# Performance work log

Hardware: AMD Instinct MI355X
Metric: run time of the kernel (lower is better)

Reference implementation:

```python
import jax, jax.numpy as jnp
import numpy as np

N, K, GDIM, DDIM, HID = 2000, 250, 256, 20, 150
GIJ = 3 * GDIM + DDIM  # 788
BINS = jnp.array([1, 2, 3, 4, 8, 16, 32, 64], dtype=jnp.int32)


def _pair_structure():
    # span i (1..N-1) has min(i, K) antecedents: spans i-L .. i-1
    lengths = np.minimum(np.arange(1, N), K)
    i_arr = np.repeat(np.arange(1, N), lengths)
    pos = np.concatenate([np.arange(L) for L in lengths])
    Lrep = np.repeat(lengths, lengths)
    j_arr = i_arr - Lrep + pos
    seg = np.repeat(np.arange(N - 1), lengths)
    # span k covers tokens [2k, 2k+1]; distance = i.i2 - j.i1
    dist = (2 * i_arr + 1) - 2 * j_arr
    return i_arr, j_arr, dist, seg, pos, lengths


def setup_inputs() -> dict:
    key = jax.random.key(0)
    ks = jax.random.split(key, 8)
    i_arr, j_arr, dist, seg, pos, lengths = _pair_structure()

    def w(k, shape, scale):
        return jax.random.normal(k, shape, dtype=jnp.float32) * scale

    return {
        "g_i": w(ks[0], (N, GDIM), 1.0),
        "mention_scores": w(ks[1], (N, 1), 1.0),
        "dist_embed": w(ks[2], (9, DDIM), 0.1),
        "W1": w(ks[3], (GIJ, HID), float(1.0 / np.sqrt(GIJ))),
        "b1": jnp.zeros((HID,), jnp.float32),
        "W2": w(ks[4], (HID, HID), float(1.0 / np.sqrt(HID))),
        "b2": jnp.zeros((HID,), jnp.float32),
        "W3": w(ks[5], (HID, 1), float(1.0 / np.sqrt(HID))),
        "b3": jnp.zeros((1,), jnp.float32),
        "mention_ids": jnp.asarray(i_arr, jnp.int32),
        "antecedent_ids": jnp.asarray(j_arr, jnp.int32),
        "distances": jnp.asarray(dist, jnp.int32),
        "seg_ids": jnp.asarray(seg, jnp.int32),
        "pos_ids": jnp.asarray(pos, jnp.int32),
        "lengths": jnp.asarray(lengths, jnp.int32),
    }


def reference(g_i, mention_scores, dist_embed, W1, b1, W2, b2, W3, b3,
              mention_ids, antecedent_ids, distances, seg_ids, pos_ids, lengths):
    # Distance.stoi: bin index = number of bins <= num; then embedding lookup
    dist_idx = jnp.sum(distances[:, None] >= BINS[None, :], axis=1)
    phi = dist_embed[dist_idx]                               # [P, DDIM]

    i_g = g_i[mention_ids]                                   # [P, GDIM]
    j_g = g_i[antecedent_ids]                                # [P, GDIM]
    pairs = jnp.concatenate([i_g, j_g, i_g * j_g, phi], axis=1)  # [P, GIJ]

    # Score MLP (dropout is identity in eval mode)
    h = jax.nn.relu(pairs @ W1 + b1)
    h = jax.nn.relu(h @ W2 + b2)
    s_ij = h @ W3 + b3                                       # [P, 1]

    coref = mention_scores[mention_ids] + mention_scores[antecedent_ids] + s_ij  # [P, 1]
    c = coref[:, 0]

    # ragged per-span softmax with appended epsilon (score 0), pad value 1000
    n_groups = lengths.shape[0]                              # N - 1 nonempty groups
    mat = jnp.full((n_groups, K + 1), -jnp.inf, dtype=c.dtype)
    mat = mat.at[seg_ids, pos_ids].set(c)
    mat = mat.at[jnp.arange(n_groups), lengths].set(0.0)     # epsilon slot
    probs_rows = jax.nn.softmax(mat, axis=1)                 # -inf -> prob 0
    valid = jnp.arange(K + 1)[None, :] <= lengths[:, None]
    probs_rows = jnp.where(valid, probs_rows, jnp.asarray(1000.0, c.dtype))
    # leading empty group: softmax([epsilon]) = [1.0], rest padded with 1000
    first = jnp.full((1, K + 1), 1000.0, dtype=c.dtype).at[0, 0].set(1.0)
    probs = jnp.concatenate([first, probs_rows], axis=0)     # [N, K+1]

    with_epsilon_my = jnp.concatenate([jnp.zeros_like(coref), coref], axis=1)  # [P, 2]
    return probs, with_epsilon_my
```

## Files before the change

kernel.cpp:

```cpp
#include <hip/hip_runtime.h>
#include <hip/hip_bf16.h>

#define GDIM 256
#define HID 150
#define HP 160
#define KMAX 250
#define NMAX 2000

typedef __attribute__((ext_vector_type(8))) short bf16x8;
typedef __attribute__((ext_vector_type(4))) float f32x4;

#define FU   0
#define FV   (FU + NMAX*HP)
#define FD   (FV + NMAX*HP)
#define FW3  (FD + 9*HP)
#define FB2  (FW3 + HP)
#define FEND (FB2 + HP)
#define CH_SH 5120
#define NCH1  8
#define NCH   13

static __device__ __forceinline__ short cvt_bf(float x) {
  __hip_bfloat16 h = __float2bfloat16(x);
  return *reinterpret_cast<short*>(&h);
}

static __device__ __forceinline__ void gl_lds16(const void* g, void* l) {
  __builtin_amdgcn_global_load_lds(
      (const __attribute__((address_space(1))) unsigned int*)g,
      (__attribute__((address_space(3))) unsigned int*)l, 16, 0, 0);
}

__global__ void precompute_uv(const float* __restrict__ g_i,
                              const float* __restrict__ W1,
                              const float* __restrict__ b1,
                              float* __restrict__ ws, int N) {
  int t = blockIdx.x * blockDim.x + threadIdx.x;
  int total = N * HP;
  bool isV = false;
  if (t >= total) { t -= total; isV = true; }
  if (t >= total) return;
  int r = t / HP, c = t - (t / HP) * HP;
  float acc = 0.f;
  if (c < HID) {
    const float* w = W1 + (isV ? GDIM * HID : 0) + c;
    const float* g = g_i + (size_t)r * GDIM;
#pragma unroll 8
    for (int k = 0; k < GDIM; k++) acc = fmaf(g[k], w[(size_t)k * HID], acc);
    if (!isV) acc += b1[c];
  }
  ws[(isV ? FV : FU) + (size_t)r * HP + c] = acc;
}

__global__ void precompute_tabs(const float* __restrict__ dist_embed,
                                const float* __restrict__ W1,
                                const float* __restrict__ W2,
                                const float* __restrict__ b2,
                                const float* __restrict__ W3,
                                float* __restrict__ wsf) {
  unsigned short* wsu = (unsigned short*)(wsf + FEND);
  int t = blockIdx.x * blockDim.x + threadIdx.x;
  if (t < 9 * HP) {
    int d = t / HP, c = t - d * HP;
    float a = 0.f;
    if (c < HID) {
#pragma unroll
      for (int k = 0; k < 20; k++)
        a = fmaf(dist_embed[d * 20 + k], W1[(size_t)(768 + k) * HID + c], a);
    }
    wsf[FD + t] = a;
    return;
  }
  t -= 9 * HP;
  if (t < HP) { wsf[FW3 + t] = (t < HID) ? W3[t] : 0.f; return; }
  t -= HP;
  if (t < HP) { wsf[FB2 + t] = (t < HID) ? b2[t] : 0.f; return; }
  t -= HP;
  if (t < NCH * CH_SH) {
    int ch = t / CH_SH, qs = t - ch * CH_SH;
    int s = qs >> 6, bs = qs & 63;
    int bbs = bs ^ ((s & 7) << 3);
    int n = 2 * s + (bbs >> 5);
    int kk = bbs & 31;
    float w = 0.f;
    if (ch < NCH1) {
      int k = ch * 32 + kk;
      if (n < HID) w = W1[(size_t)(2 * GDIM + k) * HID + n];
    } else {
      int k = (ch - NCH1) * 32 + kk;
      if (n < HID && k < HID) w = W2[(size_t)k * HID + n];
    }
    wsu[t] = (unsigned short)cvt_bf(w);
    return;
  }
}

__global__ __launch_bounds__(512, 4)
void pair_mlp(const float* __restrict__ g_i,
              const float* __restrict__ ms,
              const int* __restrict__ mid,
              const int* __restrict__ aid,
              const int* __restrict__ dist,
              const float* __restrict__ b3,
              const float* __restrict__ wsf,
              float* __restrict__ out2, int P) {
  __shared__ short Bb[2][CH_SH];
  __shared__ short Hh[8][2560];
  const unsigned short* wsu = (const unsigned short*)(wsf + FEND);

  int tid = threadIdx.x;
  int wave = tid >> 6, lane = tid & 63;
  int c = lane & 15, g = lane >> 4;
  int tbase = blockIdx.x * 128;

  int prow = tbase + wave * 16 + c;
  int pcA = (prow < P) ? prow : (P - 1);
  const float* gI = g_i + (size_t)mid[pcA] * GDIM;
  const float* gJ = g_i + (size_t)aid[pcA] * GDIM;

  int bOff[10];
#pragma unroll
  for (int ct = 0; ct < 10; ct++) {
    int n = 16 * ct + c;
    bOff[ct] = (n >> 1) * 128 + ((((n & 1) << 6) + g * 16) ^ (((n >> 1) & 7) << 4));
  }

  {
    const char* s = (const char*)(wsu);
    char* d = (char*)&Bb[0][0];
    gl_lds16(s + wave * 1024 + lane * 16, d + wave * 1024);
    if (wave < 2)
      gl_lds16(s + 8192 + wave * 1024 + lane * 16, d + 8192 + wave * 1024);
  }
  __syncthreads();

  f32x4 acc[10];
#pragma unroll
  for (int ct = 0; ct < 10; ct++) acc[ct] = (f32x4){0.f, 0.f, 0.f, 0.f};

  for (int t = 0; t < NCH1; t++) {
    {
      const char* s = (const char*)(wsu + (size_t)(t + 1) * CH_SH);
      char* d = (char*)&Bb[(t + 1) & 1][0];
      gl_lds16(s + wave * 1024 + lane * 16, d + wave * 1024);
      if (wave < 2)
        gl_lds16(s + 8192 + wave * 1024 + lane * 16, d + 8192 + wave * 1024);
    }
    int ko = t * 32 + g * 8;
    float4 i0 = *(const float4*)(gI + ko), i1 = *(const float4*)(gI + ko + 4);
    float4 j0 = *(const float4*)(gJ + ko), j1 = *(const float4*)(gJ + ko + 4);
    bf16x8 A;
    A[0] = cvt_bf(i0.x * j0.x); A[1] = cvt_bf(i0.y * j0.y);
    A[2] = cvt_bf(i0.z * j0.z); A[3] = cvt_bf(i0.w * j0.w);
    A[4] = cvt_bf(i1.x * j1.x); A[5] = cvt_bf(i1.y * j1.y);
    A[6] = cvt_bf(i1.z * j1.z); A[7] = cvt_bf(i1.w * j1.w);

    const char* Bp = (const char*)&Bb[t & 1][0];
#pragma unroll
    for (int ct = 0; ct < 10; ct++) {
      bf16x8 Bf = *(const bf16x8*)(Bp + bOff[ct]);
      acc[ct] = __builtin_amdgcn_mfma_f32_16x16x32_bf16(A, Bf, acc[ct], 0, 0, 0);
    }
    __syncthreads();
  }

  int im[4], jm[4], dm[4];
#pragma unroll
  for (int r = 0; r < 4; r++) {
    int p = tbase + wave * 16 + g * 4 + r;
    int pc = (p < P) ? p : (P - 1);
    im[r] = mid[pc]; jm[r] = aid[pc];
    int d = dist[pc];
    dm[r] = (d >= 1) + (d >= 2) + (d >= 3) + (d >= 4) +
            (d >= 8) + (d >= 16) + (d >= 32) + (d >= 64);
  }
  const float* Ut = wsf + FU;
  const float* Vt = wsf + FV;
  const float* Dt = wsf + FD;
  char* Hw = (char*)&Hh[wave][0];
#pragma unroll
  for (int ct = 0; ct < 10; ct++) {
#pragma unroll
    for (int r = 0; r < 4; r++) {
      int col = 16 * ct + c;
      float bias = Ut[(size_t)im[r] * HP + col] +
                   Vt[(size_t)jm[r] * HP + col] +
                   Dt[dm[r] * HP + col];
      float h = fmaxf(acc[ct][r] + bias, 0.f);
      int row = g * 4 + r;
      int byte = 32 * ct + 2 * c;
      int bo = (byte < 256) ? (byte ^ ((row & 7) << 4))
                            : (256 + ((byte - 256) ^ ((row & 3) << 4)));
      *(short*)(Hw + row * 320 + bo) = cvt_bf(h);
    }
  }

  f32x4 acc2[10];
#pragma unroll
  for (int ct = 0; ct < 10; ct++) acc2[ct] = (f32x4){0.f, 0.f, 0.f, 0.f};

  for (int t = NCH1; t < NCH; t++) {
    if (t + 1 < NCH) {
      const char* s = (const char*)(wsu + (size_t)(t + 1) * CH_SH);
      char* d = (char*)&Bb[(t + 1) & 1][0];
      gl_lds16(s + wave * 1024 + lane * 16, d + wave * 1024);
      if (wave < 2)
        gl_lds16(s + 8192 + wave * 1024 + lane * 16, d + 8192 + wave * 1024);
    }
    int ks = t - NCH1;
    int kbyte = ks * 64 + g * 16;
    int bo = (kbyte < 256) ? (kbyte ^ ((c & 7) << 4))
                           : (256 + ((kbyte - 256) ^ ((c & 3) << 4)));
    bf16x8 A2 = *(const bf16x8*)((const char*)&Hh[wave][0] + c * 320 + bo);

    const char* Bp = (const char*)&Bb[t & 1][0];
#pragma unroll
    for (int ct = 0; ct < 10; ct++) {
      bf16x8 Bf = *(const bf16x8*)(Bp + bOff[ct]);
      acc2[ct] = __builtin_amdgcn_mfma_f32_16x16x32_bf16(A2, Bf, acc2[ct], 0, 0, 0);
    }
    __syncthreads();
  }

  float b2v[10], w3v[10];
#pragma unroll
  for (int ct = 0; ct < 10; ct++) {
    b2v[ct] = wsf[FB2 + 16 * ct + c];
    w3v[ct] = wsf[FW3 + 16 * ct + c];
  }
  float b3v = b3[0];
#pragma unroll
  for (int r = 0; r < 4; r++) {
    float s = 0.f;
#pragma unroll
    for (int ct = 0; ct < 10; ct++) {
      float a = acc2[ct][r] + b2v[ct];
      s = fmaf(fmaxf(a, 0.f), w3v[ct], s);
    }
    s += __shfl_xor(s, 1, 64);
    s += __shfl_xor(s, 2, 64);
    s += __shfl_xor(s, 4, 64);
    s += __shfl_xor(s, 8, 64);
    if (c == 0) {
      int p = tbase + wave * 16 + g * 4 + r;
      if (p < P) {
        float val = s + ms[im[r]] + ms[jm[r]] + b3v;
        ((float2*)out2)[p] = make_float2(0.f, val);
      }
    }
  }
}

__global__ __launch_bounds__(64, 1)
void softmax_rows(const float* __restrict__ out2,
                  float* __restrict__ probs, int G) {
  int b = blockIdx.x;
  int t = threadIdx.x;
  if (b == 0) {
    for (int pos = t; pos <= KMAX; pos += 64)
      probs[pos] = (pos == 0) ? 1.0f : 1000.0f;
    return;
  }
  int g = b - 1;
  int L = (g + 1 < KMAX) ? g + 1 : KMAX;
  int base = (g <= KMAX) ? g * (g + 1) / 2
                         : KMAX * (KMAX + 1) / 2 + (g - KMAX) * KMAX;
  float mx = 0.f;
  for (int pos = t; pos < L; pos += 64)
    mx = fmaxf(mx, out2[2 * (base + pos) + 1]);
#pragma unroll
  for (int off = 32; off >= 1; off >>= 1) mx = fmaxf(mx, __shfl_xor(mx, off));

  float sum = (t == 0) ? expf(-mx) : 0.f;
  for (int pos = t; pos < L; pos += 64)
    sum += expf(out2[2 * (base + pos) + 1] - mx);
#pragma unroll
  for (int off = 32; off >= 1; off >>= 1) sum += __shfl_xor(sum, off);
  float inv = 1.f / sum;

  float* row = probs + (size_t)(g + 1) * (KMAX + 1);
  for (int pos = t; pos <= KMAX; pos += 64) {
    float v;
    if (pos < L)       v = expf(out2[2 * (base + pos) + 1] - mx) * inv;
    else if (pos == L) v = expf(-mx) * inv;
    else               v = 1000.0f;
    row[pos] = v;
  }
}

extern "C" void kernel_launch(void* const* d_in, const int* in_sizes, int n_in,
                              void* d_out, int out_size, void* d_ws, size_t ws_size,
                              hipStream_t stream) {
  const float* g_i        = (const float*)d_in[0];
  const float* ms         = (const float*)d_in[1];
  const float* dist_embed = (const float*)d_in[2];
  const float* W1         = (const float*)d_in[3];
  const float* b1         = (const float*)d_in[4];
  const float* W2         = (const float*)d_in[5];
  const float* b2         = (const float*)d_in[6];
  const float* W3         = (const float*)d_in[7];
  const float* b3         = (const float*)d_in[8];
  const int* mid          = (const int*)d_in[9];
  const int* aid          = (const int*)d_in[10];
  const int* dist         = (const int*)d_in[11];

  int N = in_sizes[0] / GDIM;
  int P = in_sizes[9];
  int G = in_sizes[14];

  float* wsf   = (float*)d_ws;
  float* probs = (float*)d_out;
  float* out2  = (float*)d_out + (size_t)(G + 1) * (KMAX + 1);

  int tot_uv = 2 * N * HP;
  precompute_uv<<<(tot_uv + 255) / 256, 256, 0, stream>>>(g_i, W1, b1, wsf, N);
  int tot_tab = 9 * HP + 2 * HP + NCH * CH_SH;
  precompute_tabs<<<(tot_tab + 255) / 256, 256, 0, stream>>>(dist_embed, W1, W2, b2, W3, wsf);
  pair_mlp<<<(P + 127) / 128, 512, 0, stream>>>(g_i, ms, mid, aid, dist, b3, wsf, out2, P);
  softmax_rows<<<G + 1, 64, 0, stream>>>(out2, probs, G);
}
```

Before: 352.7 us.

## Give each wave two M tiles with K=64 chunks and register prefetch

The pair MLP kernel moves from 8 waves that each own 16 rows to 4 waves that each own 32 rows (two M tiles), so every B fragment read from LDS feeds two MFMAs. Weight chunks grow to K=64 with a new swizzle, which halves the number of barrier-separated steps. The next chunk's g_i rows are prefetched into registers, and the MFMA loops are wrapped in s_setprio. precompute_uv also computes four columns per thread. The trade-off is higher register pressure and lower occupancy (256 threads, launch bounds 2), which may hurt latency hiding of the gather loads.

Result: faster. 295.8 us (-16.1%).

```diff
diff --git a/kernel.cpp b/kernel.cpp
--- a/kernel.cpp
+++ b/kernel.cpp
@@ -16,9 +16,8 @@
 #define FW3  (FD + 9*HP)
 #define FB2  (FW3 + HP)
 #define FEND (FB2 + HP)
-#define CH_SH 5120
-#define NCH1  8
-#define NCH   13
+#define CHFULL 10240
+#define UBTOT  66560
 
 static __device__ __forceinline__ short cvt_bf(float x) {
   __hip_bfloat16 h = __float2bfloat16(x);
@@ -29,6 +28,14 @@
   __builtin_amdgcn_global_load_lds(
       (const __attribute__((address_space(1))) unsigned int*)g,
       (__attribute__((address_space(3))) unsigned int*)l, 16, 0, 0);
+}
+
+static __device__ __forceinline__ void stage_chunk(const unsigned short* src, short* dst,
+                                                   int nseg, int wave, int lane) {
+  const char* s = (const char*)src;
+  char* d = (char*)dst;
+  for (int seg = wave; seg < nseg; seg += 4)
+    gl_lds16(s + seg * 1024 + lane * 16, d + seg * 1024);
 }
 
 __global__ void precompute_uv(const float* __restrict__ g_i,
@@ -36,20 +43,36 @@
                               const float* __restrict__ b1,
                               float* __restrict__ ws, int N) {
   int t = blockIdx.x * blockDim.x + threadIdx.x;
-  int total = N * HP;
+  int total = N * (HP / 4);
   bool isV = false;
   if (t >= total) { t -= total; isV = true; }
   if (t >= total) return;
-  int r = t / HP, c = t - (t / HP) * HP;
-  float acc = 0.f;
-  if (c < HID) {
-    const float* w = W1 + (isV ? GDIM * HID : 0) + c;
+  int r = t / (HP / 4), c4 = (t - r * (HP / 4)) * 4;
+  float a0 = 0.f, a1 = 0.f, a2 = 0.f, a3 = 0.f;
+  if (c4 < HID) {
+    const float* w = W1 + (isV ? GDIM * HID : 0) + c4;
     const float* g = g_i + (size_t)r * GDIM;
-#pragma unroll 8
-    for (int k = 0; k < GDIM; k++) acc = fmaf(g[k], w[(size_t)k * HID], acc);
-    if (!isV) acc += b1[c];
-  }
-  ws[(isV ? FV : FU) + (size_t)r * HP + c] = acc;
+#pragma unroll 4
+    for (int k = 0; k < GDIM; k++) {
+      float gv = g[k];
+      const float* wr = w + (size_t)k * HID;
+      a0 = fmaf(gv, wr[0], a0);
+      a1 = fmaf(gv, wr[1], a1);
+      a2 = fmaf(gv, wr[2], a2);
+      a3 = fmaf(gv, wr[3], a3);
+    }
+    if (!isV) {
+      a0 += b1[c4];
+      if (c4 + 1 < HID) a1 += b1[c4 + 1];
+      if (c4 + 2 < HID) a2 += b1[c4 + 2];
+      if (c4 + 3 < HID) a3 += b1[c4 + 3];
+    }
+  }
+  float* dst = ws + (isV ? FV : FU) + (size_t)r * HP + c4;
+  dst[0] = (c4     < HID) ? a0 : 0.f;
+  dst[1] = (c4 + 1 < HID) ? a1 : 0.f;
+  dst[2] = (c4 + 2 < HID) ? a2 : 0.f;
+  dst[3] = (c4 + 3 < HID) ? a3 : 0.f;
 }
 
 __global__ void precompute_tabs(const float* __restrict__ dist_embed,
@@ -76,18 +99,19 @@
   t -= HP;
   if (t < HP) { wsf[FB2 + t] = (t < HID) ? b2[t] : 0.f; return; }
   t -= HP;
-  if (t < NCH * CH_SH) {
-    int ch = t / CH_SH, qs = t - ch * CH_SH;
-    int s = qs >> 6, bs = qs & 63;
-    int bbs = bs ^ ((s & 7) << 3);
-    int n = 2 * s + (bbs >> 5);
-    int kk = bbs & 31;
+  if (t < UBTOT) {
+    int ch, s;
+    if (t < 6 * CHFULL) { ch = t / CHFULL; s = t - ch * CHFULL; }
+    else                { ch = 6; s = t - 6 * CHFULL; }
+    int n, kl;
+    if (ch < 6) { n = s >> 6; kl = (s & 63) ^ ((n & 7) << 3); }
+    else        { n = s >> 5; kl = (s & 31) ^ ((n & 3) << 3); }
     float w = 0.f;
-    if (ch < NCH1) {
-      int k = ch * 32 + kk;
+    if (ch < 4) {
+      int k = ch * 64 + kl;
       if (n < HID) w = W1[(size_t)(2 * GDIM + k) * HID + n];
     } else {
-      int k = (ch - NCH1) * 32 + kk;
+      int k = (ch - 4) * 64 + kl;
       if (n < HID && k < HID) w = W2[(size_t)k * HID + n];
     }
     wsu[t] = (unsigned short)cvt_bf(w);
@@ -95,7 +119,7 @@
   }
 }
 
-__global__ __launch_bounds__(512, 4)
+__global__ __launch_bounds__(256, 2)
 void pair_mlp(const float* __restrict__ g_i,
               const float* __restrict__ ms,
               const int* __restrict__ mid,
@@ -104,122 +128,188 @@
               const float* __restrict__ b3,
               const float* __restrict__ wsf,
               float* __restrict__ out2, int P) {
-  __shared__ short Bb[2][CH_SH];
-  __shared__ short Hh[8][2560];
-  const unsigned short* wsu = (const unsigned short*)(wsf + FEND);
+  __shared__ short Bb[2][CHFULL];
+  __shared__ short Hh[4][5120];
+  const unsigned short* UB = (const unsigned short*)(wsf + FEND);
 
   int tid = threadIdx.x;
   int wave = tid >> 6, lane = tid & 63;
   int c = lane & 15, g = lane >> 4;
-  int tbase = blockIdx.x * 128;
-
-  int prow = tbase + wave * 16 + c;
-  int pcA = (prow < P) ? prow : (P - 1);
-  const float* gI = g_i + (size_t)mid[pcA] * GDIM;
-  const float* gJ = g_i + (size_t)aid[pcA] * GDIM;
-
-  int bOff[10];
-#pragma unroll
-  for (int ct = 0; ct < 10; ct++) {
-    int n = 16 * ct + c;
-    bOff[ct] = (n >> 1) * 128 + ((((n & 1) << 6) + g * 16) ^ (((n >> 1) & 7) << 4));
-  }
-
-  {
-    const char* s = (const char*)(wsu);
-    char* d = (char*)&Bb[0][0];
-    gl_lds16(s + wave * 1024 + lane * 16, d + wave * 1024);
-    if (wave < 2)
-      gl_lds16(s + 8192 + wave * 1024 + lane * 16, d + 8192 + wave * 1024);
-  }
+  int tbase = blockIdx.x * 128 + wave * 32;
+
+  int p0 = tbase + c;      if (p0 >= P) p0 = P - 1;
+  int p1 = tbase + 16 + c; if (p1 >= P) p1 = P - 1;
+  const float* gI0 = g_i + (size_t)mid[p0] * GDIM;
+  const float* gJ0 = g_i + (size_t)aid[p0] * GDIM;
+  const float* gI1 = g_i + (size_t)mid[p1] * GDIM;
+  const float* gJ1 = g_i + (size_t)aid[p1] * GDIM;
+
+  int xr7 = (c & 7) << 4;
+  int xr3 = (c & 3) << 4;
+  int nb[10];
+#pragma unroll
+  for (int ct = 0; ct < 10; ct++) nb[ct] = (16 * ct + c) * 128;
+  int ko[2] = { (g * 16) ^ xr7, (64 + g * 16) ^ xr7 };
+
+  float pfv[64];
+  bf16x8 Af[2][2];
+
+#define PF_LOAD(T) do {                                                        \
+    int kb = (T) * 64 + g * 8;                                                 \
+    _Pragma("unroll")                                                          \
+    for (int mt = 0; mt < 2; mt++) {                                           \
+      const float* pi = mt ? gI1 : gI0;                                        \
+      const float* pj = mt ? gJ1 : gJ0;                                        \
+      _Pragma("unroll")                                                        \
+      for (int k2 = 0; k2 < 2; k2++) {                                         \
+        int kk = kb + k2 * 32;                                                 \
+        int bs = (mt * 2 + k2) * 16;                                           \
+        *(float4*)&pfv[bs + 0]  = *(const float4*)(pi + kk);                   \
+        *(float4*)&pfv[bs + 4]  = *(const float4*)(pi + kk + 4);               \
+        *(float4*)&pfv[bs + 8]  = *(const float4*)(pj + kk);                   \
+        *(float4*)&pfv[bs + 12] = *(const float4*)(pj + kk + 4);               \
+      }                                                                        \
+    }                                                                          \
+  } while (0)
+
+#define PF_CVT() do {                                                          \
+    _Pragma("unroll")                                                          \
+    for (int mt = 0; mt < 2; mt++)                                             \
+    _Pragma("unroll")                                                          \
+    for (int k2 = 0; k2 < 2; k2++) {                                           \
+      int bs = (mt * 2 + k2) * 16;                                             \
+      _Pragma("unroll")                                                        \
+      for (int e = 0; e < 8; e++)                                              \
+        Af[mt][k2][e] = cvt_bf(pfv[bs + e] * pfv[bs + 8 + e]);                 \
+    }                                                                          \
+  } while (0)
+
+  PF_LOAD(0);
+  stage_chunk(UB, &Bb[0][0], 20, wave, lane);
   __syncthreads();
 
-  f32x4 acc[10];
-#pragma unroll
-  for (int ct = 0; ct < 10; ct++) acc[ct] = (f32x4){0.f, 0.f, 0.f, 0.f};
-
-  for (int t = 0; t < NCH1; t++) {
-    {
-      const char* s = (const char*)(wsu + (size_t)(t + 1) * CH_SH);
-      char* d = (char*)&Bb[(t + 1) & 1][0];
-      gl_lds16(s + wave * 1024 + lane * 16, d + wave * 1024);
-      if (wave < 2)
-        gl_lds16(s + 8192 + wave * 1024 + lane * 16, d + 8192 + wave * 1024);
-    }
-    int ko = t * 32 + g * 8;
-    float4 i0 = *(const float4*)(gI + ko), i1 = *(const float4*)(gI + ko + 4);
-    float4 j0 = *(const float4*)(gJ + ko), j1 = *(const float4*)(gJ + ko + 4);
-    bf16x8 A;
-    A[0] = cvt_bf(i0.x * j0.x); A[1] = cvt_bf(i0.y * j0.y);
-    A[2] = cvt_bf(i0.z * j0.z); A[3] = cvt_bf(i0.w * j0.w);
-    A[4] = cvt_bf(i1.x * j1.x); A[5] = cvt_bf(i1.y * j1.y);
-    A[6] = cvt_bf(i1.z * j1.z); A[7] = cvt_bf(i1.w * j1.w);
-
+  f32x4 acc[2][10];
+#pragma unroll
+  for (int mt = 0; mt < 2; mt++)
+#pragma unroll
+    for (int ct = 0; ct < 10; ct++) acc[mt][ct] = (f32x4){0.f, 0.f, 0.f, 0.f};
+
+#pragma unroll
+  for (int t = 0; t < 4; t++) {
+    PF_CVT();
+    if (t < 3) PF_LOAD(t + 1);
+    stage_chunk(UB + (size_t)(t + 1) * CHFULL, &Bb[(t + 1) & 1][0], 20, wave, lane);
     const char* Bp = (const char*)&Bb[t & 1][0];
-#pragma unroll
-    for (int ct = 0; ct < 10; ct++) {
-      bf16x8 Bf = *(const bf16x8*)(Bp + bOff[ct]);
-      acc[ct] = __builtin_amdgcn_mfma_f32_16x16x32_bf16(A, Bf, acc[ct], 0, 0, 0);
-    }
+    __builtin_amdgcn_s_setprio(1);
+#pragma unroll
+    for (int k2 = 0; k2 < 2; k2++)
+#pragma unroll
+      for (int ct = 0; ct < 10; ct++) {
+        bf16x8 Bf = *(const bf16x8*)(Bp + nb[ct] + ko[k2]);
+        acc[0][ct] = __builtin_amdgcn_mfma_f32_16x16x32_bf16(Af[0][k2], Bf, acc[0][ct], 0, 0, 0);
+        acc[1][ct] = __builtin_amdgcn_mfma_f32_16x16x32_bf16(Af[1][k2], Bf, acc[1][ct], 0, 0, 0);
+      }
+    __builtin_amdgcn_s_setprio(0);
     __syncthreads();
   }
 
-  int im[4], jm[4], dm[4];
-#pragma unroll
-  for (int r = 0; r < 4; r++) {
-    int p = tbase + wave * 16 + g * 4 + r;
-    int pc = (p < P) ? p : (P - 1);
-    im[r] = mid[pc]; jm[r] = aid[pc];
-    int d = dist[pc];
-    dm[r] = (d >= 1) + (d >= 2) + (d >= 3) + (d >= 4) +
-            (d >= 8) + (d >= 16) + (d >= 32) + (d >= 64);
-  }
+  int im[2][4], jm[2][4], dm[2][4];
+#pragma unroll
+  for (int mt = 0; mt < 2; mt++)
+#pragma unroll
+    for (int r = 0; r < 4; r++) {
+      int p = tbase + mt * 16 + 4 * g + r;
+      int pc = (p < P) ? p : (P - 1);
+      im[mt][r] = mid[pc]; jm[mt][r] = aid[pc];
+      int d = dist[pc];
+      dm[mt][r] = (d >= 1) + (d >= 2) + (d >= 3) + (d >= 4) +
+                  (d >= 8) + (d >= 16) + (d >= 32) + (d >= 64);
+    }
   const float* Ut = wsf + FU;
   const float* Vt = wsf + FV;
   const float* Dt = wsf + FD;
   char* Hw = (char*)&Hh[wave][0];
 #pragma unroll
-  for (int ct = 0; ct < 10; ct++) {
-#pragma unroll
-    for (int r = 0; r < 4; r++) {
-      int col = 16 * ct + c;
-      float bias = Ut[(size_t)im[r] * HP + col] +
-                   Vt[(size_t)jm[r] * HP + col] +
-                   Dt[dm[r] * HP + col];
-      float h = fmaxf(acc[ct][r] + bias, 0.f);
-      int row = g * 4 + r;
-      int byte = 32 * ct + 2 * c;
-      int bo = (byte < 256) ? (byte ^ ((row & 7) << 4))
-                            : (256 + ((byte - 256) ^ ((row & 3) << 4)));
-      *(short*)(Hw + row * 320 + bo) = cvt_bf(h);
-    }
-  }
-
-  f32x4 acc2[10];
-#pragma unroll
-  for (int ct = 0; ct < 10; ct++) acc2[ct] = (f32x4){0.f, 0.f, 0.f, 0.f};
-
-  for (int t = NCH1; t < NCH; t++) {
-    if (t + 1 < NCH) {
-      const char* s = (const char*)(wsu + (size_t)(t + 1) * CH_SH);
-      char* d = (char*)&Bb[(t + 1) & 1][0];
-      gl_lds16(s + wave * 1024 + lane * 16, d + wave * 1024);
-      if (wave < 2)
-        gl_lds16(s + 8192 + wave * 1024 + lane * 16, d + 8192 + wave * 1024);
-    }
-    int ks = t - NCH1;
-    int kbyte = ks * 64 + g * 16;
-    int bo = (kbyte < 256) ? (kbyte ^ ((c & 7) << 4))
-                           : (256 + ((kbyte - 256) ^ ((c & 3) << 4)));
-    bf16x8 A2 = *(const bf16x8*)((const char*)&Hh[wave][0] + c * 320 + bo);
-
-    const char* Bp = (const char*)&Bb[t & 1][0];
+  for (int mt = 0; mt < 2; mt++)
+#pragma unroll
+    for (int ct = 0; ct < 10; ct++)
+#pragma unroll
+      for (int r = 0; r < 4; r++) {
+        int col = 16 * ct + c;
+        float bias = Ut[(size_t)im[mt][r] * HP + col] +
+                     Vt[(size_t)jm[mt][r] * HP + col] +
+                     Dt[dm[mt][r] * HP + col];
+        float h = fmaxf(acc[mt][ct][r] + bias, 0.f);
+        int row = mt * 16 + 4 * g + r;
+        int byte = 32 * ct + 2 * c;
+        int bo = (byte < 256) ? (byte ^ ((row & 7) << 4))
+                              : (256 + ((byte - 256) ^ ((row & 3) << 4)));
+        *(short*)(Hw + row * 320 + bo) = cvt_bf(h);
+      }
+
+  f32x4 acc2[2][10];
+#pragma unroll
+  for (int mt = 0; mt < 2; mt++)
+#pragma unroll
+    for (int ct = 0; ct < 10; ct++) acc2[mt][ct] = (f32x4){0.f, 0.f, 0.f, 0.f};
+
+  const char* Hc = (const char*)&Hh[wave][0];
+  bf16x8 A2[2][2];
+
+#define H_FRAG(MT, K2, KS) do {                                                \
+    int row = (MT) * 16 + c;                                                   \
+    int byte = (KS) * 128 + (K2) * 64 + g * 16;                                \
+    int bo = (byte < 256) ? (byte ^ ((row & 7) << 4))                          \
+                          : (256 + ((byte - 256) ^ ((row & 3) << 4)));         \
+    A2[MT][K2] = *(const bf16x8*)(Hc + row * 320 + bo);                        \
+  } while (0)
+
+  stage_chunk(UB + (size_t)5 * CHFULL, &Bb[1][0], 20, wave, lane);
+  H_FRAG(0, 0, 0); H_FRAG(0, 1, 0); H_FRAG(1, 0, 0); H_FRAG(1, 1, 0);
+  {
+    const char* Bp = (const char*)&Bb[0][0];
+    __builtin_amdgcn_s_setprio(1);
+#pragma unroll
+    for (int k2 = 0; k2 < 2; k2++)
+#pragma unroll
+      for (int ct = 0; ct < 10; ct++) {
+        bf16x8 Bf = *(const bf16x8*)(Bp + nb[ct] + ko[k2]);
+        acc2[0][ct] = __builtin_amdgcn_mfma_f32_16x16x32_bf16(A2[0][k2], Bf, acc2[0][ct], 0, 0, 0);
+        acc2[1][ct] = __builtin_amdgcn_mfma_f32_16x16x32_bf16(A2[1][k2], Bf, acc2[1][ct], 0, 0, 0);
+      }
+    __builtin_amdgcn_s_setprio(0);
+  }
+  __syncthreads();
+
+  stage_chunk(UB + (size_t)6 * CHFULL, &Bb[0][0], 10, wave, lane);
+  H_FRAG(0, 0, 1); H_FRAG(0, 1, 1); H_FRAG(1, 0, 1); H_FRAG(1, 1, 1);
+  {
+    const char* Bp = (const char*)&Bb[1][0];
+    __builtin_amdgcn_s_setprio(1);
+#pragma unroll
+    for (int k2 = 0; k2 < 2; k2++)
+#pragma unroll
+      for (int ct = 0; ct < 10; ct++) {
+        bf16x8 Bf = *(const bf16x8*)(Bp + nb[ct] + ko[k2]);
+        acc2[0][ct] = __builtin_amdgcn_mfma_f32_16x16x32_bf16(A2[0][k2], Bf, acc2[0][ct], 0, 0, 0);
+        acc2[1][ct] = __builtin_amdgcn_mfma_f32_16x16x32_bf16(A2[1][k2], Bf, acc2[1][ct], 0, 0, 0);
+      }
+    __builtin_amdgcn_s_setprio(0);
+  }
+  __syncthreads();
+
+  H_FRAG(0, 0, 2); H_FRAG(1, 0, 2);
+  {
+    const char* Bp = (const char*)&Bb[0][0];
+    int koT = (g * 16) ^ xr3;
+    __builtin_amdgcn_s_setprio(1);
 #pragma unroll
     for (int ct = 0; ct < 10; ct++) {
-      bf16x8 Bf = *(const bf16x8*)(Bp + bOff[ct]);
-      acc2[ct] = __builtin_amdgcn_mfma_f32_16x16x32_bf16(A2, Bf, acc2[ct], 0, 0, 0);
-    }
-    __syncthreads();
+      bf16x8 Bf = *(const bf16x8*)(Bp + (16 * ct + c) * 64 + koT);
+      acc2[0][ct] = __builtin_amdgcn_mfma_f32_16x16x32_bf16(A2[0][0], Bf, acc2[0][ct], 0, 0, 0);
+      acc2[1][ct] = __builtin_amdgcn_mfma_f32_16x16x32_bf16(A2[1][0], Bf, acc2[1][ct], 0, 0, 0);
+    }
+    __builtin_amdgcn_s_setprio(0);
   }
 
   float b2v[10], w3v[10];
@@ -230,25 +320,30 @@
   }
   float b3v = b3[0];
 #pragma unroll
-  for (int r = 0; r < 4; r++) {
-    float s = 0.f;
-#pragma unroll
-    for (int ct = 0; ct < 10; ct++) {
-      float a = acc2[ct][r] + b2v[ct];
-      s = fmaf(fmaxf(a, 0.f), w3v[ct], s);
-    }
-    s += __shfl_xor(s, 1, 64);
-    s += __shfl_xor(s, 2, 64);
-    s += __shfl_xor(s, 4, 64);
-    s += __shfl_xor(s, 8, 64);
-    if (c == 0) {
-      int p = tbase + wave * 16 + g * 4 + r;
-      if (p < P) {
-        float val = s + ms[im[r]] + ms[jm[r]] + b3v;
-        ((float2*)out2)[p] = make_float2(0.f, val);
-      }
-    }
-  }
+  for (int mt = 0; mt < 2; mt++)
+#pragma unroll
+    for (int r = 0; r < 4; r++) {
+      float s = 0.f;
+#pragma unroll
+      for (int ct = 0; ct < 10; ct++) {
+        float a = acc2[mt][ct][r] + b2v[ct];
+        s = fmaf(fmaxf(a, 0.f), w3v[ct], s);
+      }
+      s += __shfl_xor(s, 1, 64);
+      s += __shfl_xor(s, 2, 64);
+      s += __shfl_xor(s, 4, 64);
+      s += __shfl_xor(s, 8, 64);
+      if (c == 0) {
+        int p = tbase + mt * 16 + 4 * g + r;
+        if (p < P) {
+          float val = s + ms[im[mt][r]] + ms[jm[mt][r]] + b3v;
+          ((float2*)out2)[p] = make_float2(0.f, val);
+        }
+      }
+    }
+#undef PF_LOAD
+#undef PF_CVT
+#undef H_FRAG
 }
 
 __global__ __launch_bounds__(64, 1)
@@ -312,10 +407,10 @@
   float* probs = (float*)d_out;
   float* out2  = (float*)d_out + (size_t)(G + 1) * (KMAX + 1);
 
-  int tot_uv = 2 * N * HP;
+  int tot_uv = 2 * N * (HP / 4);
   precompute_uv<<<(tot_uv + 255) / 256, 256, 0, stream>>>(g_i, W1, b1, wsf, N);
-  int tot_tab = 9 * HP + 2 * HP + NCH * CH_SH;
+  int tot_tab = 9 * HP + 2 * HP + UBTOT;
   precompute_tabs<<<(tot_tab + 255) / 256, 256, 0, stream>>>(dist_embed, W1, W2, b2, W3, wsf);
-  pair_mlp<<<(P + 127) / 128, 512, 0, stream>>>(g_i, ms, mid, aid, dist, b3, wsf, out2, P);
+  pair_mlp<<<(P + 127) / 128, 256, 0, stream>>>(g_i, ms, mid, aid, dist, b3, wsf, out2, P);
   softmax_rows<<<G + 1, 64, 0, stream>>>(out2, probs, G);
 }
```
